# Kernel optimization log

Measured on AMD Instinct MI355X. Metric: run time of the kernel, lower is better.

Reference implementation:

```python
import jax, jax.numpy as jnp
import numpy as np

# SPU activation from the RAI-2021 project: x^2 - 0.5 for x>=0, sigmoid(-x)-1 for x<0.

def spu(x):
    s = jax.nn.sigmoid(-x)
    return jnp.where(x >= 0, x * x - 0.5, s - 1.0)

def dspu(x):
    s = jax.nn.sigmoid(-x)
    return jnp.where(x >= 0, 2.0 * x, -s * (1.0 - s))

def get_homog(w, b):
    # [[w, b], [0, 1]]: maps coeff rows over layer outputs (out+1) -> coeffs over inputs (in+1)
    top = jnp.concatenate([w, b[:, None]], axis=1)
    bot = jnp.concatenate([jnp.zeros((1, w.shape[1]), w.dtype), jnp.ones((1, 1), w.dtype)], axis=1)
    return jnp.concatenate([top, bot], axis=0)

def slope_clip(l, u, w_l, w_u):
    # clip slopes into the range spanned by SPU derivatives at the interval endpoints
    k1, k2 = dspu(l), dspu(u)
    klo, khi = jnp.minimum(k1, k2), jnp.maximum(k1, k2)
    return jnp.clip(w_l, klo, khi), jnp.clip(w_u, klo, khi)

def lb_slope(l, u, w_l, w_u):
    # intercepts so that w*x+b lower/upper bounds SPU at the probe points {l, u, mid, 0}
    pts = jnp.stack([l, u, 0.5 * (l + u), jnp.clip(0.0, l, u)], axis=0)  # [4, n]
    b_l = jnp.min(spu(pts) - w_l[None, :] * pts, axis=0)
    b_u = jnp.max(spu(pts) - w_u[None, :] * pts, axis=0)
    return b_l, b_u

def back_sub(Wl, Wu, affine):
    # vectorized back-substitution: the per-row torch.where matmul collapses to
    # relu(l)@W_l + min(l,0)@W_u (and symmetrically for u)
    l, u = Wl[-1], Wu[-1]
    for i in range(len(Wl) - 2, -1, -1):
        if affine[i]:
            l = l @ Wl[i]
            u = u @ Wl[i]
        else:
            l = jnp.maximum(l, 0.0) @ Wl[i] + jnp.minimum(l, 0.0) @ Wu[i]
            u = jnp.maximum(u, 0.0) @ Wu[i] + jnp.minimum(u, 0.0) @ Wl[i]
    return l, u

def _forward(W1, b1, W2, b2, W3, b3, W4, b4, l_in, u_in,
             p_l1, p_u1, p_l2, p_u2, p_l3, p_u3, true_label):
    dt = W1.dtype
    Ws = [get_homog(W1, b1), get_homog(W2, b2), get_homog(W3, b3), get_homog(W4, b4)]
    one = jnp.ones((1, 1), dt)
    l0 = jnp.concatenate([l_in, one], axis=0)  # [d_in+1, 1]
    u0 = jnp.concatenate([u_in, one], axis=0)
    K = Ws[-1].shape[0]  # n_out + 1
    eye = jnp.eye(K, dtype=dt)
    w_out = jnp.concatenate([eye[:true_label], eye[true_label + 1:-1]], axis=0)  # [n_out-1, n_out+1]
    w_out = w_out.at[:, true_label].add(-1.0)
    spu_params = [(p_l1, p_u1), (p_l2, p_u2), (p_l3, p_u3)]
    Wl, Wu, affine = [l0], [u0], [False]
    for i in range(len(Ws)):
        Wl.append(Ws[i]); Wu.append(Ws[i]); affine.append(True)
        if i < len(Ws) - 1:
            l, u = back_sub(Wl, Wu, affine)
            lf, uf = l[:-1, 0], u[:-1, 0]
            pl, pu = spu_params[i]
            cl, cu = slope_clip(lf, uf, pl, pu)
            # torch copies clipped values into the leaf params under no_grad -> straight-through
            wl = pl + jax.lax.stop_gradient(cl - pl)
            wu = pu + jax.lax.stop_gradient(cu - pu)
            b_l, b_u = lb_slope(lf, uf, wl, wu)
            Wl.append(get_homog(jnp.diag(wl), b_l))
            Wu.append(get_homog(jnp.diag(wu), b_u))
            affine.append(False)
    Wl.append(w_out); Wu.append(w_out); affine.append(True)
    _, u = back_sub(Wl, Wu, affine)
    return u.flatten()

def setup_inputs() -> dict:
    key = jax.random.key(0)
    ks = jax.random.split(key, 10)
    d_in, h, n_out = 784, 2048, 10
    s = 0.03
    W1 = jax.random.normal(ks[0], (h, d_in), jnp.float32) * s
    b1 = jax.random.normal(ks[1], (h,), jnp.float32) * s
    W2 = jax.random.normal(ks[2], (h, h), jnp.float32) * s
    b2 = jax.random.normal(ks[3], (h,), jnp.float32) * s
    W3 = jax.random.normal(ks[4], (h, h), jnp.float32) * s
    b3 = jax.random.normal(ks[5], (h,), jnp.float32) * s
    W4 = jax.random.normal(ks[6], (n_out, h), jnp.float32) * s
    b4 = jax.random.normal(ks[7], (n_out,), jnp.float32) * s
    x = jax.random.normal(ks[8], (d_in, 1), jnp.float32)
    eps = 0.05
    return {
        'W1': W1, 'b1': b1, 'W2': W2, 'b2': b2, 'W3': W3, 'b3': b3, 'W4': W4, 'b4': b4,
        'l_in': x - eps, 'u_in': x + eps,
        'p_l1': jnp.zeros((h,), jnp.float32), 'p_u1': jnp.zeros((h,), jnp.float32),
        'p_l2': jnp.zeros((h,), jnp.float32), 'p_u2': jnp.zeros((h,), jnp.float32),
        'p_l3': jnp.zeros((h,), jnp.float32), 'p_u3': jnp.zeros((h,), jnp.float32),
        'true_label': 3,
    }

def reference(W1, b1, W2, b2, W3, b3, W4, b4, l_in, u_in,
              p_l1, p_u1, p_l2, p_u2, p_l3, p_u3, true_label):
    return _forward(W1, b1, W2, b2, W3, b3, W4, b4, l_in, u_in,
                    p_l1, p_u1, p_l2, p_u2, p_l3, p_u3, int(true_label))
```

## Files before the change

### kernel.cpp

```cpp
#include <hip/hip_runtime.h>
#include <math.h>

#define H 2048
#define DIN 784
#define DPAD 896

typedef unsigned short ushort_t;
typedef __attribute__((ext_vector_type(8))) short bf16x8;
typedef __attribute__((ext_vector_type(4))) float f32x4;
typedef __attribute__((ext_vector_type(4))) unsigned short u16x4;
typedef __attribute__((ext_vector_type(8))) unsigned short u16x8;
union F4 { float4 v; float a[4]; };
union U4 { u16x4 v; ushort_t a[4]; };
union U8 { u16x8 v; ushort_t a[8]; };

__device__ __forceinline__ float spu_f(float x){
    if (x >= 0.0f) return x*x - 0.5f;
    float s = 1.0f / (1.0f + __expf(x));
    return s - 1.0f;
}
__device__ __forceinline__ float dspu_f(float x){
    if (x >= 0.0f) return 2.0f*x;
    float s = 1.0f / (1.0f + __expf(x));
    return -s * (1.0f - s);
}
__device__ __forceinline__ ushort_t f2bf(float x){
    unsigned u = __float_as_uint(x);
    unsigned r = (u + 0x7FFFu + ((u >> 16) & 1u)) >> 16;
    return (ushort_t)r;
}
__device__ __forceinline__ float bf2f(ushort_t h){
    return __uint_as_float((unsigned)h << 16);
}
__device__ __forceinline__ void load_lds16(const void* g, void* l){
    __builtin_amdgcn_global_load_lds((const __attribute__((address_space(1))) void*)g,
                                     (__attribute__((address_space(3))) void*)l,
                                     16, 0, 0);
}
__device__ __forceinline__ float block_reduce_256(float v, float* red){
    #pragma unroll
    for (int off = 32; off > 0; off >>= 1) v += __shfl_down(v, off, 64);
    int lane = threadIdx.x & 63, w = threadIdx.x >> 6;
    if (lane == 0) red[w] = v;
    __syncthreads();
    float t = 0.f;
    if (threadIdx.x == 0) t = red[0] + red[1] + red[2] + red[3];
    return t;
}
__device__ __forceinline__ void block_reduce2_256(float vl, float vu, float* red,
                                                  float& out_l, float& out_u){
    #pragma unroll
    for (int off = 32; off > 0; off >>= 1){
        vl += __shfl_down(vl, off, 64);
        vu += __shfl_down(vu, off, 64);
    }
    int lane = threadIdx.x & 63, w = threadIdx.x >> 6;
    if (lane == 0){ red[w] = vl; red[4 + w] = vu; }
    __syncthreads();
    if (threadIdx.x == 0){
        out_l = red[0] + red[1] + red[2] + red[3];
        out_u = red[4] + red[5] + red[6] + red[7];
    }
}
__device__ __forceinline__ void spu_relax(float l, float u, float pl, float pu,
                                          float& wl_o, float& wu_o, float& bl_o, float& bu_o){
    float k1 = dspu_f(l), k2 = dspu_f(u);
    float klo = fminf(k1, k2), khi = fmaxf(k1, k2);
    float cwl = fminf(fmaxf(pl, klo), khi);
    float cwu = fminf(fmaxf(pu, klo), khi);
    float pts[4];
    pts[0] = l; pts[1] = u; pts[2] = 0.5f*(l+u); pts[3] = fminf(fmaxf(0.f, l), u);
    float bmin = INFINITY, bmax = -INFINITY;
    #pragma unroll
    for (int t = 0; t < 4; t++){
        float sp = spu_f(pts[t]);
        bmin = fminf(bmin, sp - cwl * pts[t]);
        bmax = fmaxf(bmax, sp - cwu * pts[t]);
    }
    wl_o = cwl; wu_o = cwu; bl_o = bmin; bu_o = bmax;
}

__global__ __launch_bounds__(256) void conv_bounds1(
    const float* __restrict__ W2, ushort_t* __restrict__ T2,
    const float* __restrict__ W1, ushort_t* __restrict__ T1,
    const float* __restrict__ b1,
    const float* __restrict__ l_in, const float* __restrict__ u_in,
    const float* __restrict__ pl, const float* __restrict__ pu,
    float* __restrict__ wl, float* __restrict__ wu,
    float* __restrict__ bl, float* __restrict__ bu)
{
    int z = blockIdx.z;
    if (z < 2){
        __shared__ float tile[32][33];
        const float* W = z ? W1 : W2;
        ushort_t* T = z ? T1 : T2;
        int K = H, N = z ? DIN : H, Npad = z ? DPAD : H;
        if (blockIdx.x * 32 >= (unsigned)Npad) return;
        int n0 = blockIdx.x * 32, k0 = blockIdx.y * 32;
        int tx = threadIdx.x & 31;
        int ty = threadIdx.x >> 5;
        #pragma unroll
        for (int i = 0; i < 32; i += 8){
            int k = k0 + ty + i, n = n0 + tx;
            tile[ty + i][tx] = (k < K && n < N) ? W[(size_t)k * N + n] : 0.f;
        }
        __syncthreads();
        #pragma unroll
        for (int i = 0; i < 32; i += 8){
            int n = n0 + ty + i, k = k0 + tx;
            if (n < Npad && k < K) T[(size_t)n * K + k] = f2bf(tile[tx][ty + i]);
        }
        return;
    }
    int row = blockIdx.y * 64 + blockIdx.x;
    if (row >= H) return;
    __shared__ float red[8];
    const F4* Mr = (const F4*)(W1 + (size_t)row * DIN);
    const F4* li4 = (const F4*)l_in;
    const F4* ui4 = (const F4*)u_in;
    float accl = 0.f, accu = 0.f;
    for (int q = threadIdx.x; q < DIN/4; q += 256){
        F4 v = Mr[q], lo = li4[q], up = ui4[q];
        #pragma unroll
        for (int c = 0; c < 4; c++){
            float p = fmaxf(v.a[c], 0.f), n = fminf(v.a[c], 0.f);
            accl += p * lo.a[c] + n * up.a[c];
            accu += p * up.a[c] + n * lo.a[c];
        }
    }
    float tl, tu;
    block_reduce2_256(accl, accu, red, tl, tu);
    if (threadIdx.x == 0){
        float bb = b1[row];
        spu_relax(tl + bb, tu + bb, pl[row], pu[row],
                  wl[row], wu[row], bl[row], bu[row]);
    }
}

__global__ __launch_bounds__(256) void bounds_parts(
    const ushort_t* __restrict__ P_l, const ushort_t* __restrict__ P_u,
    const float* __restrict__ c_l, const float* __restrict__ c_u,
    const float* __restrict__ l_in, const float* __restrict__ u_in,
    const float* __restrict__ pl, const float* __restrict__ pu,
    float* __restrict__ wl, float* __restrict__ wu,
    float* __restrict__ bl, float* __restrict__ bu,
    int ncols, int ld, size_t pstride, int nparts)
{
    __shared__ float red[8];
    int row = blockIdx.x;
    const ushort_t* Ml = P_l + (size_t)row * ld;
    const ushort_t* Mu = P_u + (size_t)row * ld;
    const F4* li4 = (const F4*)l_in;
    const F4* ui4 = (const F4*)u_in;
    float accl = 0.f, accu = 0.f;
    for (int q = threadIdx.x; q < ncols/4; q += 256){
        float vl[4] = {0.f,0.f,0.f,0.f}, vu[4] = {0.f,0.f,0.f,0.f};
        for (int s = 0; s < nparts; s++){
            U4 a, b;
            a.v = *(const u16x4*)&Ml[(size_t)s * pstride + q*4];
            b.v = *(const u16x4*)&Mu[(size_t)s * pstride + q*4];
            #pragma unroll
            for (int c = 0; c < 4; c++){ vl[c] += bf2f(a.a[c]); vu[c] += bf2f(b.a[c]); }
        }
        F4 lo = li4[q], up = ui4[q];
        #pragma unroll
        for (int c = 0; c < 4; c++){
            accl += fmaxf(vl[c], 0.f) * lo.a[c] + fminf(vl[c], 0.f) * up.a[c];
            accu += fmaxf(vu[c], 0.f) * up.a[c] + fminf(vu[c], 0.f) * lo.a[c];
        }
    }
    float tl, tu;
    block_reduce2_256(accl, accu, red, tl, tu);
    if (threadIdx.x == 0){
        spu_relax(tl + c_l[row], tu + c_u[row], pl[row], pu[row],
                  wl[row], wu[row], bl[row], bu[row]);
    }
}

__global__ __launch_bounds__(256) void dapply_dual(
    const float* __restrict__ S, const float* __restrict__ c_in,
    const float* __restrict__ wl, const float* __restrict__ wu,
    const float* __restrict__ bl, const float* __restrict__ bu,
    const float* __restrict__ bias_next,
    ushort_t* __restrict__ Ml, ushort_t* __restrict__ Mu,
    float* __restrict__ cl_out, float* __restrict__ cu_out, int ncols)
{
    __shared__ float red[8];
    int row = blockIdx.x;
    const F4* S4 = (const F4*)(S + (size_t)row * ncols);
    u16x4* Ml4 = (u16x4*)(Ml + (size_t)row * ncols);
    u16x4* Mu4 = (u16x4*)(Mu + (size_t)row * ncols);
    const F4* wl4 = (const F4*)wl; const F4* wu4 = (const F4*)wu;
    const F4* bl4 = (const F4*)bl; const F4* bu4 = (const F4*)bu;
    const F4* bn4 = (const F4*)bias_next;
    float accl = 0.f, accu = 0.f;
    for (int q = threadIdx.x; q < ncols/4; q += 256){
        F4 v = S4[q], a = wl4[q], b = wu4[q], c = bl4[q], d = bu4[q], e = bn4[q];
        U4 rl, ru;
        #pragma unroll
        for (int k = 0; k < 4; k++){
            float p = fmaxf(v.a[k], 0.f), n = fminf(v.a[k], 0.f);
            float ml = p * a.a[k] + n * b.a[k];
            float mu = p * b.a[k] + n * a.a[k];
            rl.a[k] = f2bf(ml);
            ru.a[k] = f2bf(mu);
            accl += p * c.a[k] + n * d.a[k] + ml * e.a[k];
            accu += p * d.a[k] + n * c.a[k] + mu * e.a[k];
        }
        Ml4[q] = rl.v;
        Mu4[q] = ru.v;
    }
    float tl, tu;
    block_reduce2_256(accl, accu, red, tl, tu);
    if (threadIdx.x == 0){
        float cc = c_in[row];
        cl_out[row] = cc + tl;
        cu_out[row] = cc + tu;
    }
}

__global__ __launch_bounds__(256) void dapply_parts(
    const ushort_t* __restrict__ P_l, const ushort_t* __restrict__ P_u,
    const float* __restrict__ cl_in, const float* __restrict__ cu_in,
    const float* __restrict__ wl, const float* __restrict__ wu,
    const float* __restrict__ bl, const float* __restrict__ bu,
    const float* __restrict__ bias_next,
    ushort_t* __restrict__ Ml, ushort_t* __restrict__ Mu,
    float* __restrict__ cl_out, float* __restrict__ cu_out,
    int ncols, size_t pstride, int nparts)
{
    __shared__ float red[4];
    int row = blockIdx.x;
    int lu = blockIdx.y;
    const ushort_t* Sr = (lu ? P_u : P_l) + (size_t)row * ncols;
    const float* w_pos = lu ? wu : wl;
    const float* w_neg = lu ? wl : wu;
    const float* b_pos = lu ? bu : bl;
    const float* b_neg = lu ? bl : bu;
    u16x8* Mr8 = (u16x8*)((lu ? Mu : Ml) + (size_t)row * ncols);
    float acc = 0.f;
    for (int q = threadIdx.x; q < ncols/8; q += 256){
        float vv[8];
        {
            U8 t; t.v = *(const u16x8*)&Sr[q*8];
            #pragma unroll
            for (int c = 0; c < 8; c++) vv[c] = bf2f(t.a[c]);
        }
        for (int s = 1; s < nparts; s++){
            U8 t; t.v = *(const u16x8*)&Sr[(size_t)s * pstride + q*8];
            #pragma unroll
            for (int c = 0; c < 8; c++) vv[c] += bf2f(t.a[c]);
        }
        U8 r;
        #pragma unroll
        for (int c = 0; c < 8; c++){
            int j = q*8 + c;
            float p = fmaxf(vv[c], 0.f), n = fminf(vv[c], 0.f);
            float m = p * w_pos[j] + n * w_neg[j];
            r.a[c] = f2bf(m);
            acc += p * b_pos[j] + n * b_neg[j] + m * bias_next[j];
        }
        Mr8[q] = r.v;
    }
    float t = block_reduce_256(acc, red);
    if (threadIdx.x == 0){
        if (lu) cu_out[row] = cu_in[row] + t;
        else    cl_out[row] = cl_in[row] + t;
    }
}

__global__ __launch_bounds__(256) void input_reduce(
    const float* __restrict__ M, const float* __restrict__ c,
    const float* __restrict__ pos_b, const float* __restrict__ neg_b,
    float* __restrict__ out, int ncols, int ld)
{
    __shared__ float red[4];
    int row = blockIdx.x;
    const float* Mr = M + (size_t)row * ld;
    float acc = 0.f;
    for (int j = threadIdx.x; j < ncols; j += 256){
        float v = Mr[j];
        acc += fmaxf(v, 0.f) * pos_b[j] + fminf(v, 0.f) * neg_b[j];
    }
    float t = block_reduce_256(acc, red);
    if (threadIdx.x == 0) out[row] = t + c[row];
}

#define TM 128
#define TN 128
#define TK 64
__global__ __launch_bounds__(512, 4) void gemm_mfma_pair(
    const ushort_t* __restrict__ A_l, const ushort_t* __restrict__ A_u,
    const ushort_t* __restrict__ BT,
    ushort_t* __restrict__ C_l, ushort_t* __restrict__ C_u,
    int M, int N, int K, int ksplit, size_t part_stride)
{
    __shared__ ushort_t As[TM * TK];
    __shared__ ushort_t Bs[TN * TK];
    int z = blockIdx.z;
    int lu = z / ksplit, ks = z - lu * ksplit;
    const ushort_t* A = lu ? A_u : A_l;
    ushort_t* C = (lu ? C_u : C_l) + (size_t)ks * part_stride;
    int Kpart = K / ksplit;
    int kbeg = ks * Kpart;

    int tid  = threadIdx.x;
    int wave = tid >> 6, lane = tid & 63;
    int wm = (wave >> 2) * 64, wn = (wave & 3) * 32;
    int l16 = lane & 15, quad = lane >> 4;
    int row0 = blockIdx.y * TM, col0 = blockIdx.x * TN;

    int r_lo = tid >> 3;
    int kp = (((tid & 7) ^ (r_lo & 7)) * 8);
    const ushort_t *aSrc[2], *bSrc[2];
    ushort_t *aDst[2], *bDst[2];
    #pragma unroll
    for (int g = 0; g < 2; g++){
        aSrc[g] = A  + (size_t)(row0 + g*64 + r_lo) * K + kbeg + kp;
        bSrc[g] = BT + (size_t)(col0 + g*64 + r_lo) * K + kbeg + kp;
        aDst[g] = As + g*4096 + wave*512;
        bDst[g] = Bs + g*4096 + wave*512;
    }

    f32x4 acc[4][2];
    #pragma unroll
    for (int i = 0; i < 4; i++)
        #pragma unroll
        for (int j = 0; j < 2; j++)
            acc[i][j] = (f32x4){0.f, 0.f, 0.f, 0.f};

    for (int kk0 = 0; kk0 < Kpart; kk0 += TK){
        #pragma unroll
        for (int g = 0; g < 2; g++) load_lds16(aSrc[g], aDst[g]);
        #pragma unroll
        for (int g = 0; g < 2; g++) load_lds16(bSrc[g], bDst[g]);
        #pragma unroll
        for (int g = 0; g < 2; g++){ aSrc[g] += TK; bSrc[g] += TK; }
        __syncthreads();

        #pragma unroll
        for (int half = 0; half < 2; half++){
            bf16x8 af[4], bf[2];
            #pragma unroll
            for (int t = 0; t < 4; t++){
                int ra = wm + t*16 + l16;
                int sa = (half*4 + quad) ^ (ra & 7);
                af[t] = *(const bf16x8*)&As[ra * TK + sa * 8];
            }
            #pragma unroll
            for (int t = 0; t < 2; t++){
                int rb = wn + t*16 + l16;
                int sb = (half*4 + quad) ^ (rb & 7);
                bf[t] = *(const bf16x8*)&Bs[rb * TK + sb * 8];
            }
            #pragma unroll
            for (int i = 0; i < 4; i++)
                #pragma unroll
                for (int j = 0; j < 2; j++)
                    acc[i][j] = __builtin_amdgcn_mfma_f32_16x16x32_bf16(af[i], bf[j], acc[i][j], 0, 0, 0);
        }
        __syncthreads();
    }

    #pragma unroll
    for (int i = 0; i < 4; i++){
        #pragma unroll
        for (int j = 0; j < 2; j++){
            int r0 = row0 + wm + i*16 + quad*4;
            int cc = col0 + wn + j*16 + l16;
            #pragma unroll
            for (int rr = 0; rr < 4; rr++)
                C[(size_t)(r0 + rr) * N + cc] = f2bf(acc[i][j][rr]);
        }
    }
}

#define GK9 64
__global__ __launch_bounds__(64) void gemv9_fused(
    const float* __restrict__ S,
    const float* __restrict__ W4, const float* __restrict__ b4,
    const int* __restrict__ tlp, int mode_w4,
    const float* __restrict__ c_in,
    const float* __restrict__ w_pos, const float* __restrict__ w_neg,
    const float* __restrict__ b_pos, const float* __restrict__ b_neg,
    const float* __restrict__ bias_next,
    const float* __restrict__ B, int K, int N,
    float* __restrict__ C, float* __restrict__ c_out)
{
    __shared__ float Alds[9][GK9];
    int j = threadIdx.x;
    int k0 = blockIdx.y * GK9;
    int k = k0 + j;
    float wp = w_pos[k], wn = w_neg[k], bp = b_pos[k], bn = b_neg[k], bb = bias_next[k];
    int tl = mode_w4 ? *tlp : 0;
    float pc[9];
    #pragma unroll
    for (int r = 0; r < 9; r++){
        float v;
        if (mode_w4){
            int kr = r + (r >= tl ? 1 : 0);
            v = W4[(size_t)kr * K + k] - W4[(size_t)tl * K + k];
        } else {
            v = S[(size_t)r * K + k];
        }
        float p = fmaxf(v, 0.f), n = fminf(v, 0.f);
        float m = p * wp + n * wn;
        Alds[r][j] = m;
        pc[r] = p * bp + n * bn + m * bb;
    }
    if (blockIdx.x == 0){
        #pragma unroll
        for (int r = 0; r < 9; r++){
            float v = pc[r];
            #pragma unroll
            for (int o = 32; o > 0; o >>= 1) v += __shfl_down(v, o, 64);
            if (j == 0){
                if (blockIdx.y == 0)
                    v += mode_w4 ? (b4[r + (r >= tl ? 1 : 0)] - b4[tl]) : c_in[r];
                atomicAdd(&c_out[r], v);
            }
        }
    }
    __syncthreads();
    int col = blockIdx.x * GK9 + j;
    if (col < N){
        float acc[9] = {0.f,0.f,0.f,0.f,0.f,0.f,0.f,0.f,0.f};
        for (int kk = 0; kk < GK9; kk++){
            float b = B[(size_t)(k0 + kk) * N + col];
            #pragma unroll
            for (int r = 0; r < 9; r++) acc[r] += Alds[r][kk] * b;
        }
        #pragma unroll
        for (int r = 0; r < 9; r++) atomicAdd(&C[(size_t)r * N + col], acc[r]);
    }
}

extern "C" void kernel_launch(void* const* d_in, const int* in_sizes, int n_in,
                              void* d_out, int out_size, void* d_ws, size_t ws_size,
                              hipStream_t stream)
{
    const float* W1  = (const float*)d_in[0];
    const float* b1  = (const float*)d_in[1];
    const float* W2  = (const float*)d_in[2];
    const float* b2  = (const float*)d_in[3];
    const float* W3  = (const float*)d_in[4];
    const float* b3  = (const float*)d_in[5];
    const float* W4  = (const float*)d_in[6];
    const float* b4  = (const float*)d_in[7];
    const float* l_in = (const float*)d_in[8];
    const float* u_in = (const float*)d_in[9];
    const float* p_l1 = (const float*)d_in[10];
    const float* p_u1 = (const float*)d_in[11];
    const float* p_l2 = (const float*)d_in[12];
    const float* p_u2 = (const float*)d_in[13];
    const float* p_l3 = (const float*)d_in[14];
    const float* p_u3 = (const float*)d_in[15];
    const int*   tl   = (const int*)d_in[16];
    float* out = (float*)d_out;

    size_t off = 0;
    auto allocB = [&](size_t bytes) -> void* {
        void* p = (char*)d_ws + off;
        off += (bytes + 255) & ~(size_t)255;
        return p;
    };
    ushort_t* W1bt  = (ushort_t*)allocB((size_t)DPAD * H * 2);
    ushort_t* W2bt  = (ushort_t*)allocB((size_t)H * H * 2);
    ushort_t* Abf_l = (ushort_t*)allocB((size_t)H * H * 2);
    ushort_t* Abf_u = (ushort_t*)allocB((size_t)H * H * 2);
    ushort_t* P_l = (ushort_t*)allocB((size_t)2 * H * H * 2);
    ushort_t* P_u = (ushort_t*)allocB((size_t)2 * H * H * 2);
    float *wl1=(float*)allocB(H*4), *wu1=(float*)allocB(H*4), *bl1=(float*)allocB(H*4), *bu1=(float*)allocB(H*4);
    float *wl2=(float*)allocB(H*4), *wu2=(float*)allocB(H*4), *bl2=(float*)allocB(H*4), *bu2=(float*)allocB(H*4);
    float *wl3=(float*)allocB(H*4), *wu3=(float*)allocB(H*4), *bl3=(float*)allocB(H*4), *bu3=(float*)allocB(H*4);
    float *cl_a=(float*)allocB(H*4), *cl_b=(float*)allocB(H*4);
    float *cu_a=(float*)allocB(H*4), *cu_b=(float*)allocB(H*4);
    size_t zero_begin = off;
    float* F1  = (float*)allocB(9 * H * 4);
    float* F2  = (float*)allocB(9 * H * 4);
    float* F3  = (float*)allocB(9 * DIN * 4);
    float *c9b=(float*)allocB(64), *c9c=(float*)allocB(64), *c9d=(float*)allocB(64);
    size_t zero_bytes = off - zero_begin;

    const size_t ND_PART = (size_t)H * DPAD;
    const size_t NN_PART = (size_t)H * H;

    dim3 blk(256);
    dim3 gblk(512);

    hipMemsetAsync((char*)d_ws + zero_begin, 0, zero_bytes, stream);

    conv_bounds1<<<dim3(H/32, H/32, 3), blk, 0, stream>>>(
        W2, W2bt, W1, W1bt, b1, l_in, u_in, p_l1, p_u1, wl1, wu1, bl1, bu1);

    dapply_dual<<<H, blk, 0, stream>>>(W2, b2, wl1, wu1, bl1, bu1, b1,
                                       Abf_l, Abf_u, cl_a, cu_a, H);
    gemm_mfma_pair<<<dim3(DPAD/TN, H/TM, 4), gblk, 0, stream>>>(
        Abf_l, Abf_u, W1bt, P_l, P_u, H, DPAD, H, 2, ND_PART);
    bounds_parts<<<H, blk, 0, stream>>>(P_l, P_u, cl_a, cu_a, l_in, u_in, p_l2, p_u2,
                                        wl2, wu2, bl2, bu2, DIN, DPAD, ND_PART, 2);

    dapply_dual<<<H, blk, 0, stream>>>(W3, b3, wl2, wu2, bl2, bu2, b2,
                                       Abf_l, Abf_u, cl_a, cu_a, H);
    gemm_mfma_pair<<<dim3(H/TN, H/TM, 2), gblk, 0, stream>>>(
        Abf_l, Abf_u, W2bt, P_l, P_u, H, H, H, 1, NN_PART);
    dapply_parts<<<dim3(H, 2), blk, 0, stream>>>(P_l, P_u, cl_a, cu_a,
                                                 wl1, wu1, bl1, bu1, b1,
                                                 Abf_l, Abf_u, cl_b, cu_b, H, NN_PART, 1);
    gemm_mfma_pair<<<dim3(DPAD/TN, H/TM, 4), gblk, 0, stream>>>(
        Abf_l, Abf_u, W1bt, P_l, P_u, H, DPAD, H, 2, ND_PART);
    bounds_parts<<<H, blk, 0, stream>>>(P_l, P_u, cl_b, cu_b, l_in, u_in, p_l3, p_u3,
                                        wl3, wu3, bl3, bu3, DIN, DPAD, ND_PART, 2);

    gemv9_fused<<<dim3(H/GK9, H/GK9), dim3(GK9), 0, stream>>>(
        nullptr, W4, b4, tl, 1, nullptr,
        wu3, wl3, bu3, bl3, b3, W3, H, H, F1, c9b);
    gemv9_fused<<<dim3(H/GK9, H/GK9), dim3(GK9), 0, stream>>>(
        F1, nullptr, nullptr, nullptr, 0, c9b,
        wu2, wl2, bu2, bl2, b2, W2, H, H, F2, c9c);
    gemv9_fused<<<dim3((DIN + GK9 - 1)/GK9, H/GK9), dim3(GK9), 0, stream>>>(
        F2, nullptr, nullptr, nullptr, 0, c9c,
        wu1, wl1, bu1, bl1, b1, W1, H, DIN, F3, c9d);
    input_reduce<<<9, blk, 0, stream>>>(F3, c9d, u_in, l_in, out, DIN, DIN);
}
```

Before: 323.0 us.

## Fuse dapply_parts into the NN GEMM epilogue with atomic row-sum accumulation

The elementwise SPU back-substitution step (relu split, slope multiply, bias dot product) moves into the epilogue of the H×H MFMA GEMM, which writes the bf16 coefficient matrix directly. Per-row bias sums are built with shuffle reductions and atomicAdd into zeroed accumulators. The separate kernel launch and the full read and write of the intermediate 2048×2048 bf16 matrices go away. Buffers are rotated to fit this, and bounds_parts gains an optional second bias vector. The cost is atomic traffic and float-atomic ordering nondeterminism.

```diff
diff --git a/kernel.cpp b/kernel.cpp
--- a/kernel.cpp
+++ b/kernel.cpp
@@ -140,6 +140,7 @@
 __global__ __launch_bounds__(256) void bounds_parts(
     const ushort_t* __restrict__ P_l, const ushort_t* __restrict__ P_u,
     const float* __restrict__ c_l, const float* __restrict__ c_u,
+    const float* __restrict__ c_l2, const float* __restrict__ c_u2,
     const float* __restrict__ l_in, const float* __restrict__ u_in,
     const float* __restrict__ pl, const float* __restrict__ pu,
     float* __restrict__ wl, float* __restrict__ wu,
@@ -172,7 +173,9 @@
     float tl, tu;
     block_reduce2_256(accl, accu, red, tl, tu);
     if (threadIdx.x == 0){
-        spu_relax(tl + c_l[row], tu + c_u[row], pl[row], pu[row],
+        float bl_ = c_l[row] + (c_l2 ? c_l2[row] : 0.f);
+        float bu_ = c_u[row] + (c_u2 ? c_u2[row] : 0.f);
+        spu_relax(tl + bl_, tu + bu_, pl[row], pu[row],
                   wl[row], wu[row], bl[row], bu[row]);
     }
 }
@@ -219,56 +222,6 @@
     }
 }
 
-__global__ __launch_bounds__(256) void dapply_parts(
-    const ushort_t* __restrict__ P_l, const ushort_t* __restrict__ P_u,
-    const float* __restrict__ cl_in, const float* __restrict__ cu_in,
-    const float* __restrict__ wl, const float* __restrict__ wu,
-    const float* __restrict__ bl, const float* __restrict__ bu,
-    const float* __restrict__ bias_next,
-    ushort_t* __restrict__ Ml, ushort_t* __restrict__ Mu,
-    float* __restrict__ cl_out, float* __restrict__ cu_out,
-    int ncols, size_t pstride, int nparts)
-{
-    __shared__ float red[4];
-    int row = blockIdx.x;
-    int lu = blockIdx.y;
-    const ushort_t* Sr = (lu ? P_u : P_l) + (size_t)row * ncols;
-    const float* w_pos = lu ? wu : wl;
-    const float* w_neg = lu ? wl : wu;
-    const float* b_pos = lu ? bu : bl;
-    const float* b_neg = lu ? bl : bu;
-    u16x8* Mr8 = (u16x8*)((lu ? Mu : Ml) + (size_t)row * ncols);
-    float acc = 0.f;
-    for (int q = threadIdx.x; q < ncols/8; q += 256){
-        float vv[8];
-        {
-            U8 t; t.v = *(const u16x8*)&Sr[q*8];
-            #pragma unroll
-            for (int c = 0; c < 8; c++) vv[c] = bf2f(t.a[c]);
-        }
-        for (int s = 1; s < nparts; s++){
-            U8 t; t.v = *(const u16x8*)&Sr[(size_t)s * pstride + q*8];
-            #pragma unroll
-            for (int c = 0; c < 8; c++) vv[c] += bf2f(t.a[c]);
-        }
-        U8 r;
-        #pragma unroll
-        for (int c = 0; c < 8; c++){
-            int j = q*8 + c;
-            float p = fmaxf(vv[c], 0.f), n = fminf(vv[c], 0.f);
-            float m = p * w_pos[j] + n * w_neg[j];
-            r.a[c] = f2bf(m);
-            acc += p * b_pos[j] + n * b_neg[j] + m * bias_next[j];
-        }
-        Mr8[q] = r.v;
-    }
-    float t = block_reduce_256(acc, red);
-    if (threadIdx.x == 0){
-        if (lu) cu_out[row] = cu_in[row] + t;
-        else    cl_out[row] = cl_in[row] + t;
-    }
-}
-
 __global__ __launch_bounds__(256) void input_reduce(
     const float* __restrict__ M, const float* __restrict__ c,
     const float* __restrict__ pos_b, const float* __restrict__ neg_b,
@@ -371,6 +324,114 @@
             #pragma unroll
             for (int rr = 0; rr < 4; rr++)
                 C[(size_t)(r0 + rr) * N + cc] = f2bf(acc[i][j][rr]);
+        }
+    }
+}
+
+__global__ __launch_bounds__(512, 4) void gemm_nn_fused(
+    const ushort_t* __restrict__ A_l, const ushort_t* __restrict__ A_u,
+    const ushort_t* __restrict__ BT,
+    ushort_t* __restrict__ O_l, ushort_t* __restrict__ O_u,
+    const float* __restrict__ wl1, const float* __restrict__ wu1,
+    const float* __restrict__ bl1, const float* __restrict__ bu1,
+    const float* __restrict__ b1,
+    float* __restrict__ cacc_l, float* __restrict__ cacc_u,
+    int M, int N, int K)
+{
+    __shared__ ushort_t As[TM * TK];
+    __shared__ ushort_t Bs[TN * TK];
+    int lu = blockIdx.z;
+    const ushort_t* A = lu ? A_u : A_l;
+    ushort_t* O = lu ? O_u : O_l;
+    float* cacc = lu ? cacc_u : cacc_l;
+    const float* wp_a = lu ? wu1 : wl1;
+    const float* wn_a = lu ? wl1 : wu1;
+    const float* bp_a = lu ? bu1 : bl1;
+    const float* bn_a = lu ? bl1 : bu1;
+
+    int tid  = threadIdx.x;
+    int wave = tid >> 6, lane = tid & 63;
+    int wm = (wave >> 2) * 64, wn = (wave & 3) * 32;
+    int l16 = lane & 15, quad = lane >> 4;
+    int row0 = blockIdx.y * TM, col0 = blockIdx.x * TN;
+
+    int r_lo = tid >> 3;
+    int kp = (((tid & 7) ^ (r_lo & 7)) * 8);
+    const ushort_t *aSrc[2], *bSrc[2];
+    ushort_t *aDst[2], *bDst[2];
+    #pragma unroll
+    for (int g = 0; g < 2; g++){
+        aSrc[g] = A  + (size_t)(row0 + g*64 + r_lo) * K + kp;
+        bSrc[g] = BT + (size_t)(col0 + g*64 + r_lo) * K + kp;
+        aDst[g] = As + g*4096 + wave*512;
+        bDst[g] = Bs + g*4096 + wave*512;
+    }
+
+    f32x4 acc[4][2];
+    #pragma unroll
+    for (int i = 0; i < 4; i++)
+        #pragma unroll
+        for (int j = 0; j < 2; j++)
+            acc[i][j] = (f32x4){0.f, 0.f, 0.f, 0.f};
+
+    for (int kk0 = 0; kk0 < K; kk0 += TK){
+        #pragma unroll
+        for (int g = 0; g < 2; g++) load_lds16(aSrc[g], aDst[g]);
+        #pragma unroll
+        for (int g = 0; g < 2; g++) load_lds16(bSrc[g], bDst[g]);
+        #pragma unroll
+        for (int g = 0; g < 2; g++){ aSrc[g] += TK; bSrc[g] += TK; }
+        __syncthreads();
+
+        #pragma unroll
+        for (int half = 0; half < 2; half++){
+            bf16x8 af[4], bf[2];
+            #pragma unroll
+            for (int t = 0; t < 4; t++){
+                int ra = wm + t*16 + l16;
+                int sa = (half*4 + quad) ^ (ra & 7);
+                af[t] = *(const bf16x8*)&As[ra * TK + sa * 8];
+            }
+            #pragma unroll
+            for (int t = 0; t < 2; t++){
+                int rb = wn + t*16 + l16;
+                int sb = (half*4 + quad) ^ (rb & 7);
+                bf[t] = *(const bf16x8*)&Bs[rb * TK + sb * 8];
+            }
+            #pragma unroll
+            for (int i = 0; i < 4; i++)
+                #pragma unroll
+                for (int j = 0; j < 2; j++)
+                    acc[i][j] = __builtin_amdgcn_mfma_f32_16x16x32_bf16(af[i], bf[j], acc[i][j], 0, 0, 0);
+        }
+        __syncthreads();
+    }
+
+    int cc0 = col0 + wn + l16;
+    int cc1 = cc0 + 16;
+    float wp0 = wp_a[cc0], wn0 = wn_a[cc0], bp0 = bp_a[cc0], bn0 = bn_a[cc0], bb0 = b1[cc0];
+    float wp1 = wp_a[cc1], wn1 = wn_a[cc1], bp1 = bp_a[cc1], bn1 = bn_a[cc1], bb1 = b1[cc1];
+    #pragma unroll
+    for (int i = 0; i < 4; i++){
+        int rbase = row0 + wm + i*16 + quad*4;
+        #pragma unroll
+        for (int rr = 0; rr < 4; rr++){
+            int r = rbase + rr;
+            float v0 = acc[i][0][rr];
+            float p0 = fmaxf(v0, 0.f), n0 = fminf(v0, 0.f);
+            float m0 = p0 * wp0 + n0 * wn0;
+            O[(size_t)r * N + cc0] = f2bf(m0);
+            float s = p0 * bp0 + n0 * bn0 + m0 * bb0;
+            float v1 = acc[i][1][rr];
+            float p1 = fmaxf(v1, 0.f), n1 = fminf(v1, 0.f);
+            float m1 = p1 * wp1 + n1 * wn1;
+            O[(size_t)r * N + cc1] = f2bf(m1);
+            s += p1 * bp1 + n1 * bn1 + m1 * bb1;
+            s += __shfl_down(s, 8, 16);
+            s += __shfl_down(s, 4, 16);
+            s += __shfl_down(s, 2, 16);
+            s += __shfl_down(s, 1, 16);
+            if (l16 == 0) atomicAdd(&cacc[r], s);
         }
     }
 }
@@ -466,16 +527,16 @@
     };
     ushort_t* W1bt  = (ushort_t*)allocB((size_t)DPAD * H * 2);
     ushort_t* W2bt  = (ushort_t*)allocB((size_t)H * H * 2);
-    ushort_t* Abf_l = (ushort_t*)allocB((size_t)H * H * 2);
-    ushort_t* Abf_u = (ushort_t*)allocB((size_t)H * H * 2);
+    ushort_t* Abf_l = (ushort_t*)allocB((size_t)2 * H * H * 2);
+    ushort_t* Abf_u = (ushort_t*)allocB((size_t)2 * H * H * 2);
     ushort_t* P_l = (ushort_t*)allocB((size_t)2 * H * H * 2);
     ushort_t* P_u = (ushort_t*)allocB((size_t)2 * H * H * 2);
     float *wl1=(float*)allocB(H*4), *wu1=(float*)allocB(H*4), *bl1=(float*)allocB(H*4), *bu1=(float*)allocB(H*4);
     float *wl2=(float*)allocB(H*4), *wu2=(float*)allocB(H*4), *bl2=(float*)allocB(H*4), *bu2=(float*)allocB(H*4);
     float *wl3=(float*)allocB(H*4), *wu3=(float*)allocB(H*4), *bl3=(float*)allocB(H*4), *bu3=(float*)allocB(H*4);
-    float *cl_a=(float*)allocB(H*4), *cl_b=(float*)allocB(H*4);
-    float *cu_a=(float*)allocB(H*4), *cu_b=(float*)allocB(H*4);
+    float *cl_a=(float*)allocB(H*4), *cu_a=(float*)allocB(H*4);
     size_t zero_begin = off;
+    float *cl_b=(float*)allocB(H*4), *cu_b=(float*)allocB(H*4);
     float* F1  = (float*)allocB(9 * H * 4);
     float* F2  = (float*)allocB(9 * H * 4);
     float* F3  = (float*)allocB(9 * DIN * 4);
@@ -483,7 +544,6 @@
     size_t zero_bytes = off - zero_begin;
 
     const size_t ND_PART = (size_t)H * DPAD;
-    const size_t NN_PART = (size_t)H * H;
 
     dim3 blk(256);
     dim3 gblk(512);
@@ -497,19 +557,19 @@
                                        Abf_l, Abf_u, cl_a, cu_a, H);
     gemm_mfma_pair<<<dim3(DPAD/TN, H/TM, 4), gblk, 0, stream>>>(
         Abf_l, Abf_u, W1bt, P_l, P_u, H, DPAD, H, 2, ND_PART);
-    bounds_parts<<<H, blk, 0, stream>>>(P_l, P_u, cl_a, cu_a, l_in, u_in, p_l2, p_u2,
+    bounds_parts<<<H, blk, 0, stream>>>(P_l, P_u, cl_a, cu_a, nullptr, nullptr,
+                                        l_in, u_in, p_l2, p_u2,
                                         wl2, wu2, bl2, bu2, DIN, DPAD, ND_PART, 2);
 
     dapply_dual<<<H, blk, 0, stream>>>(W3, b3, wl2, wu2, bl2, bu2, b2,
                                        Abf_l, Abf_u, cl_a, cu_a, H);
-    gemm_mfma_pair<<<dim3(H/TN, H/TM, 2), gblk, 0, stream>>>(
-        Abf_l, Abf_u, W2bt, P_l, P_u, H, H, H, 1, NN_PART);
-    dapply_parts<<<dim3(H, 2), blk, 0, stream>>>(P_l, P_u, cl_a, cu_a,
-                                                 wl1, wu1, bl1, bu1, b1,
-                                                 Abf_l, Abf_u, cl_b, cu_b, H, NN_PART, 1);
+    gemm_nn_fused<<<dim3(H/TN, H/TM, 2), gblk, 0, stream>>>(
+        Abf_l, Abf_u, W2bt, P_l, P_u,
+        wl1, wu1, bl1, bu1, b1, cl_b, cu_b, H, H, H);
     gemm_mfma_pair<<<dim3(DPAD/TN, H/TM, 4), gblk, 0, stream>>>(
-        Abf_l, Abf_u, W1bt, P_l, P_u, H, DPAD, H, 2, ND_PART);
-    bounds_parts<<<H, blk, 0, stream>>>(P_l, P_u, cl_b, cu_b, l_in, u_in, p_l3, p_u3,
+        P_l, P_u, W1bt, Abf_l, Abf_u, H, DPAD, H, 2, ND_PART);
+    bounds_parts<<<H, blk, 0, stream>>>(Abf_l, Abf_u, cl_b, cu_b, cl_a, cu_a,
+                                        l_in, u_in, p_l3, p_u3,
                                         wl3, wu3, bl3, bu3, DIN, DPAD, ND_PART, 2);
 
     gemv9_fused<<<dim3(H/GK9, H/GK9), dim3(GK9), 0, stream>>>(
```

After: 317.6 us. Within noise of the previous version (-1.7%).
